# Kernel optimization log

Measured on AMD Instinct MI355X. Metric: run time of the kernel, lower is better.

Reference implementation:

```python
import jax, jax.numpy as jnp
import numpy as np

C_QKV = 1024
C_HIDDEN = 64
NUM_HEADS = 16
INF = 1e9


def setup_inputs() -> dict:
    key = jax.random.key(0)
    ks = jax.random.split(key, 10)
    B, S = 2, 2048
    d = C_QKV
    hd = C_HIDDEN * NUM_HEADS
    sc = 0.02
    return {
        "input_qkv": jax.random.normal(ks[0], (B, S, d), jnp.float32),
        "mask": jnp.ones((B, 1, 1, S), jnp.float32),
        "bias": jax.random.normal(ks[1], (1, NUM_HEADS, S, S), jnp.float32) * sc,
        "wq": jax.random.normal(ks[2], (d, hd), jnp.float32) * sc,
        "wk": jax.random.normal(ks[3], (d, hd), jnp.float32) * sc,
        "wv": jax.random.normal(ks[4], (d, hd), jnp.float32) * sc,
        "wg": jax.random.normal(ks[5], (d, hd), jnp.float32) * sc,
        "bg": jnp.zeros((hd,), jnp.float32),
        "wo": jax.random.normal(ks[6], (hd, d), jnp.float32) * sc,
        "bo": jnp.zeros((d,), jnp.float32),
    }


def reference(input_qkv, mask, bias, wq, wk, wv, wg, bg, wo, bo):
    B, S, _ = input_qkv.shape
    H, C = NUM_HEADS, C_HIDDEN
    # projections -> [B, H, S, C]
    q = (input_qkv @ wq).reshape(B, S, H, C).transpose(0, 2, 1, 3)
    k = (input_qkv @ wk).reshape(B, S, H, C).transpose(0, 2, 1, 3)
    v = (input_qkv @ wv).reshape(B, S, H, C).transpose(0, 2, 1, 3)
    q = q / jnp.asarray(C, q.dtype) ** 0.5
    # scores [B, H, S, S] with additive mask and pair bias
    a = jnp.einsum("bhqc,bhkc->bhqk", q, k)
    a = a + (mask - 1.0) * INF + bias
    a = jax.nn.softmax(a, axis=-1)
    o = jnp.einsum("bhqk,bhkc->bhqc", a, v).transpose(0, 2, 1, 3)  # [B,S,H,C]
    gate = jax.nn.sigmoid(input_qkv @ wg + bg).reshape(B, S, H, C)
    o = (o * gate).reshape(B, S, H * C)
    return o @ wo + bo
```

## Files before the change

### kernel.cpp

```cpp
#include <hip/hip_runtime.h>
#include <hip/hip_bf16.h>
#include <stdint.h>

typedef unsigned short u16;
typedef __attribute__((ext_vector_type(8))) short short8;
typedef __attribute__((ext_vector_type(4))) short short4v;
typedef __attribute__((ext_vector_type(4))) float f32x4;

#define MFMA16 __builtin_amdgcn_mfma_f32_16x16x32_bf16

#define GLOAD_LDS16(gsrc, ldst) \
  __builtin_amdgcn_global_load_lds((const __attribute__((address_space(1))) void*)(gsrc), \
                                   (__attribute__((address_space(3))) void*)(ldst), 16, 0, 0)

__device__ __forceinline__ u16 f2bf(float x) {
  union { float f; uint32_t u; } v; v.f = x;
  uint32_t r = v.u + 0x7FFFu + ((v.u >> 16) & 1u);
  return (u16)(r >> 16);
}
__device__ __forceinline__ u16 f2bf_rn(float x) {
  __hip_bfloat16 h = __float2bfloat16(x);
  return *reinterpret_cast<u16*>(&h);
}
__device__ __forceinline__ float bf2f(u16 b) {
  union { uint32_t u; float f; } v; v.u = ((uint32_t)b) << 16;
  return v.f;
}

__global__ __launch_bounds__(256) void convert_bf16_kernel(
    const float* __restrict__ in, u16* __restrict__ out, int n) {
  int i = (blockIdx.x * 256 + threadIdx.x) * 8;
  if (i >= n) return;
  float4 a = *(const float4*)(in + i);
  float4 b = *(const float4*)(in + i + 4);
  short8 t;
  t[0] = (short)f2bf(a.x); t[1] = (short)f2bf(a.y);
  t[2] = (short)f2bf(a.z); t[3] = (short)f2bf(a.w);
  t[4] = (short)f2bf(b.x); t[5] = (short)f2bf(b.y);
  t[6] = (short)f2bf(b.z); t[7] = (short)f2bf(b.w);
  *(short8*)(out + i) = t;
}

__global__ __launch_bounds__(256) void transpose_w64(
    const float* __restrict__ W, u16* __restrict__ WT, int KK, int NN) {
  __shared__ float tile[64][68];
  const int t = threadIdx.x;
  const int k0 = blockIdx.x * 64, n0 = blockIdx.y * 64;
  {
    int r = t >> 2, c0 = (t & 3) * 16;
    const float* src = W + (size_t)(k0 + r) * NN + n0 + c0;
#pragma unroll
    for (int j = 0; j < 16; j += 4) {
      float4 v = *(const float4*)(src + j);
      tile[r][c0 + j + 0] = v.x; tile[r][c0 + j + 1] = v.y;
      tile[r][c0 + j + 2] = v.z; tile[r][c0 + j + 3] = v.w;
    }
  }
  __syncthreads();
  {
    int n = t >> 2, kq = (t & 3) * 16;
    short8 t0, t1;
#pragma unroll
    for (int j = 0; j < 8; ++j)  t0[j] = (short)f2bf(tile[kq + j][n]);
#pragma unroll
    for (int j = 0; j < 8; ++j)  t1[j] = (short)f2bf(tile[kq + 8 + j][n]);
    u16* dst = WT + (size_t)(n0 + n) * KK + k0 + kq;
    *(short8*)dst = t0;
    *(short8*)(dst + 8) = t1;
  }
}

__global__ __launch_bounds__(256) void transpose_v64(
    const u16* __restrict__ vin, u16* __restrict__ vout) {
  __shared__ u16 tile[64][80];
  const int t = threadIdx.x;
  const int s0 = blockIdx.x * 64;
  const int bh = blockIdx.y;
  const int b = bh >> 4, h = bh & 15;
  {
    int r = t >> 2, c0 = (t & 3) * 16;
    const u16* src = vin + (size_t)(b * 2048 + s0 + r) * 1024 + h * 64 + c0;
    *(short8*)&tile[r][c0] = *(const short8*)src;
    *(short8*)&tile[r][c0 + 8] = *(const short8*)(src + 8);
  }
  __syncthreads();
  {
    int c = t >> 2, s4 = (t & 3) * 16;
    short8 t0, t1;
#pragma unroll
    for (int j = 0; j < 8; ++j) t0[j] = (short)tile[s4 + j][c];
#pragma unroll
    for (int j = 0; j < 8; ++j) t1[j] = (short)tile[s4 + 8 + j][c];
    u16* dst = vout + (size_t)(bh * 64 + c) * 2048 + s0 + s4;
    *(short8*)dst = t0;
    *(short8*)(dst + 8) = t1;
  }
}

__global__ __launch_bounds__(256) void gemm_bt128(
    const u16* __restrict__ A, const u16* __restrict__ BTbase,
    void* __restrict__ dstbase, const float* __restrict__ bvec, int mode) {
  const int K = 1024;
  const int tid = threadIdx.x, lane = tid & 63, w = tid >> 6;
  const int wr = w >> 1, wc = w & 1;
  const int l15 = lane & 15, lg = lane >> 4;
  const int z = (mode < 0) ? (int)blockIdx.z : mode;
  const u16* BT = (mode < 0) ? BTbase + (size_t)z * 1024 * 1024 : BTbase;
  const int rbase = blockIdx.x * 128;
  const int nbase = blockIdx.y * 128;
  __shared__ u16 lsA[128 * 64];
  __shared__ u16 lsB[128 * 64];
  f32x4 acc[4][4] = {};
  const int col8 = (lane & 7) * 8;
  for (int kt = 0; kt < K / 64; ++kt) {
#pragma unroll
    for (int i = 0; i < 4; ++i) {
      int row = w * 32 + i * 8 + (lane >> 3);
      const u16* sa = A + (size_t)(rbase + row) * K + kt * 64 + col8;
      GLOAD_LDS16(sa, lsA + (w * 32 + i * 8) * 64 + lane * 8);
      const u16* sb = BT + (size_t)(nbase + row) * K + kt * 64 + col8;
      GLOAD_LDS16(sb, lsB + (w * 32 + i * 8) * 64 + lane * 8);
    }
    __syncthreads();
#pragma unroll
    for (int kk = 0; kk < 2; ++kk) {
      short8 af[4], bfr[4];
#pragma unroll
      for (int m = 0; m < 4; ++m)
        af[m] = *(const short8*)&lsA[(wr * 64 + m * 16 + l15) * 64 + kk * 32 + lg * 8];
#pragma unroll
      for (int n = 0; n < 4; ++n)
        bfr[n] = *(const short8*)&lsB[(wc * 64 + n * 16 + l15) * 64 + kk * 32 + lg * 8];
#pragma unroll
      for (int m = 0; m < 4; ++m)
#pragma unroll
        for (int n = 0; n < 4; ++n)
          acc[m][n] = MFMA16(af[m], bfr[n], acc[m][n], 0, 0, 0);
    }
    __syncthreads();
  }
  const int r0 = rbase + wr * 64;
  const int c0 = nbase + wc * 64;
  if (z == 4) {
    float* out = (float*)dstbase;
#pragma unroll
    for (int m = 0; m < 4; ++m)
#pragma unroll
      for (int n = 0; n < 4; ++n)
#pragma unroll
        for (int i = 0; i < 4; ++i) {
          int r = r0 + m * 16 + lg * 4 + i;
          int c = c0 + n * 16 + l15;
          out[(size_t)r * 1024 + c] = acc[m][n][i] + bvec[c];
        }
  } else {
    u16* dq = (u16*)dstbase + (size_t)z * 4096 * 1024;
#pragma unroll
    for (int m = 0; m < 4; ++m)
#pragma unroll
      for (int n = 0; n < 4; ++n)
#pragma unroll
        for (int i = 0; i < 4; ++i) {
          int r = r0 + m * 16 + lg * 4 + i;
          int c = c0 + n * 16 + l15;
          float v = acc[m][n][i];
          if (z == 0) v *= 0.125f;
          else if (z == 3) v = 1.f / (1.f + __expf(-(v + bvec[c])));
          dq[(size_t)r * 1024 + c] = f2bf(v);
        }
  }
}

__global__ __launch_bounds__(256, 3) void attn_kernel(
    const u16* __restrict__ qws, const u16* __restrict__ kws,
    const u16* __restrict__ vt, const u16* __restrict__ gws,
    const float* __restrict__ bias, const float* __restrict__ mask,
    u16* __restrict__ og) {
  const int tid = threadIdx.x;
  const int lane = tid & 63;
  const int w = tid >> 6;
  const int l15 = lane & 15, lg = lane >> 4;
  const int bx = blockIdx.x;
  const int qt = (bx & 7) | ((bx >> 4) << 3);
  const int b = (bx >> 3) & 1;
  const int h = blockIdx.y;

  __shared__ __align__(16) u16 ring[3][4096];
  __shared__ __align__(16) u16 lsP[4][1280];
  __shared__ __align__(16) u16 lsM[2048];

  const float* bias_base = bias + ((size_t)h * 2048 + qt * 128) * 2048;
  const u16* vt_base = vt + (size_t)((b * 16 + h) * 64) * 2048;
  const u16* k_base = kws + (size_t)(b * 2048) * 1024 + h * 64;

  {
    float4 m0 = *(const float4*)(mask + b * 2048 + tid * 8);
    float4 m1 = *(const float4*)(mask + b * 2048 + tid * 8 + 4);
    short8 mm;
    mm[0] = (short)f2bf((m0.x - 1.f) * 1e9f); mm[1] = (short)f2bf((m0.y - 1.f) * 1e9f);
    mm[2] = (short)f2bf((m0.z - 1.f) * 1e9f); mm[3] = (short)f2bf((m0.w - 1.f) * 1e9f);
    mm[4] = (short)f2bf((m1.x - 1.f) * 1e9f); mm[5] = (short)f2bf((m1.y - 1.f) * 1e9f);
    mm[6] = (short)f2bf((m1.z - 1.f) * 1e9f); mm[7] = (short)f2bf((m1.w - 1.f) * 1e9f);
    *(short8*)&lsM[tid * 8] = mm;
  }

  const size_t qrow0 = (size_t)(b * 2048 + qt * 128 + w * 32 + l15) * 1024 + h * 64;
  const size_t qrow1 = qrow0 + 16 * 1024;
  short8 qf00 = *(const short8*)(qws + qrow0 + lg * 8);
  short8 qf01 = *(const short8*)(qws + qrow0 + 32 + lg * 8);
  short8 qf10 = *(const short8*)(qws + qrow1 + lg * 8);
  short8 qf11 = *(const short8*)(qws + qrow1 + 32 + lg * 8);
  asm volatile("" :: "v"(qf00), "v"(qf01), "v"(qf10), "v"(qf11));
  asm volatile("s_waitcnt vmcnt(0)" ::: "memory");

  f32x4 O[2][4] = {};
  float lacc0 = 0.f, lacc1 = 0.f;
  f32x4 bA0, bA1, bA2, bA3, bB0, bB1, bB2, bB3;

#define STAGE_KV(SLOT, KW) {                                                        \
    int r_ = tid >> 3, cg_ = tid & 7;                                               \
    GLOAD_LDS16(k_base + (size_t)((KW) * 32 + r_) * 1024 + ((cg_ ^ (r_ & 7)) * 8),  \
                &ring[SLOT][tid * 8]);                                              \
    int c_ = tid >> 2, kg_ = tid & 3;                                               \
    int sw_ = (c_ & 3) ^ ((c_ >> 2) & 3);                                           \
    GLOAD_LDS16(vt_base + (size_t)c_ * 2048 + (KW) * 32 + ((kg_ ^ sw_) * 8),        \
                &ring[SLOT][2048 + tid * 8]); }

#define BIAS_ISSUE(R0, R1, R2, R3, KW) {                                            \
    const float* bp_ = bias_base + (size_t)(w * 32 + l15) * 2048 + (KW) * 32 + lg * 4; \
    asm volatile("global_load_dwordx4 %0, %1, off" : "=v"(R0) : "v"(bp_));          \
    asm volatile("global_load_dwordx4 %0, %1, off" : "=v"(R1) : "v"(bp_ + 16));     \
    asm volatile("global_load_dwordx4 %0, %1, off" : "=v"(R2) : "v"(bp_ + 16 * 2048)); \
    asm volatile("global_load_dwordx4 %0, %1, off" : "=v"(R3) : "v"(bp_ + 16 * 2048 + 16)); \
  }

#define COMPUTE(SLOT, KB, BR00, BR01, BR10, BR11) {                                 \
    const u16* Kc_ = &ring[SLOT][0];                                                \
    const u16* Vc_ = &ring[SLOT][2048];                                             \
    const int sw_ = l15 & 7;                                                        \
    short8 kf0a = *(const short8*)&Kc_[(l15) * 64 + ((lg ^ sw_) * 8)];              \
    short8 kf0b = *(const short8*)&Kc_[(l15) * 64 + (((4 + lg) ^ sw_) * 8)];        \
    short8 kf1a = *(const short8*)&Kc_[(16 + l15) * 64 + ((lg ^ sw_) * 8)];         \
    short8 kf1b = *(const short8*)&Kc_[(16 + l15) * 64 + (((4 + lg) ^ sw_) * 8)];   \
    short4v mk0 = *(const short4v*)&lsM[(KB) * 32 + lg * 4];                        \
    short4v mk1 = *(const short4v*)&lsM[(KB) * 32 + 16 + lg * 4];                   \
    f32x4 ci00, ci01, ci10, ci11;                                                   \
    _Pragma("unroll") for (int i = 0; i < 4; ++i) {                                 \
      float m0_ = bf2f((u16)mk0[i]), m1_ = bf2f((u16)mk1[i]);                       \
      ci00[i] = BR00[i] + m0_; ci01[i] = BR01[i] + m1_;                             \
      ci10[i] = BR10[i] + m0_; ci11[i] = BR11[i] + m1_;                             \
    }                                                                               \
    f32x4 s00 = MFMA16(kf0a, qf00, ci00, 0, 0, 0);                                 \
    s00 = MFMA16(kf0b, qf01, s00, 0, 0, 0);                                         \
    f32x4 s01 = MFMA16(kf1a, qf00, ci01, 0, 0, 0);                                 \
    s01 = MFMA16(kf1b, qf01, s01, 0, 0, 0);                                         \
    f32x4 s10 = MFMA16(kf0a, qf10, ci10, 0, 0, 0);                                 \
    s10 = MFMA16(kf0b, qf11, s10, 0, 0, 0);                                         \
    f32x4 s11 = MFMA16(kf1a, qf10, ci11, 0, 0, 0);                                 \
    s11 = MFMA16(kf1b, qf11, s11, 0, 0, 0);                                         \
    short4v p00, p01, p10, p11;                                                     \
    _Pragma("unroll") for (int i = 0; i < 4; ++i) {                                 \
      float e00 = __expf(s00[i]); lacc0 += e00; p00[i] = (short)f2bf_rn(e00);       \
      float e01 = __expf(s01[i]); lacc0 += e01; p01[i] = (short)f2bf_rn(e01);       \
      float e10 = __expf(s10[i]); lacc1 += e10; p10[i] = (short)f2bf_rn(e10);       \
      float e11 = __expf(s11[i]); lacc1 += e11; p11[i] = (short)f2bf_rn(e11);       \
    }                                                                               \
    *(short4v*)&lsP[w][(l15) * 40 + lg * 4] = p00;                                  \
    *(short4v*)&lsP[w][(l15) * 40 + 16 + lg * 4] = p01;                             \
    *(short4v*)&lsP[w][(16 + l15) * 40 + lg * 4] = p10;                             \
    *(short4v*)&lsP[w][(16 + l15) * 40 + 16 + lg * 4] = p11;                        \
    short8 pf0 = *(const short8*)&lsP[w][(l15) * 40 + lg * 8];                      \
    short8 pf1 = *(const short8*)&lsP[w][(16 + l15) * 40 + lg * 8];                 \
    _Pragma("unroll") for (int cf = 0; cf < 4; ++cf) {                              \
      int c_ = cf * 16 + l15;                                                       \
      short8 vf_ = *(const short8*)&Vc_[c_ * 32 +                                   \
                                        ((lg ^ ((c_ & 3) ^ ((c_ >> 2) & 3))) * 8)]; \
      O[0][cf] = MFMA16(vf_, pf0, O[0][cf], 0, 0, 0);                               \
      O[1][cf] = MFMA16(vf_, pf1, O[1][cf], 0, 0, 0);                               \
    } }

#define BODY(KB, X0, X1, X2, X3, Y0, Y1, Y2, Y3) {                                  \
    if ((KB) + 2 < 64) STAGE_KV(((KB) + 2) % 3, (KB) + 2);                          \
    COMPUTE((KB) % 3, KB, X0, X1, X2, X3);                                          \
    if ((KB) + 2 < 64) {                                                            \
      BIAS_ISSUE(X0, X1, X2, X3, (KB) + 2);                                         \
      asm volatile("s_waitcnt vmcnt(6)" ::: "memory");                              \
    } else {                                                                        \
      asm volatile("s_waitcnt vmcnt(0)" ::: "memory");                              \
    }                                                                               \
    asm volatile("s_waitcnt lgkmcnt(0)" ::: "memory");                              \
    __builtin_amdgcn_sched_barrier(0);                                              \
    __builtin_amdgcn_s_barrier(); }

  STAGE_KV(0, 0);
  BIAS_ISSUE(bA0, bA1, bA2, bA3, 0);
  STAGE_KV(1, 1);
  BIAS_ISSUE(bB0, bB1, bB2, bB3, 1);
  asm volatile("s_waitcnt vmcnt(6)" ::: "memory");
  asm volatile("s_waitcnt lgkmcnt(0)" ::: "memory");
  __builtin_amdgcn_sched_barrier(0);
  __builtin_amdgcn_s_barrier();

  for (int kb2 = 0; kb2 < 64; kb2 += 2) {
    BODY(kb2,     bA0, bA1, bA2, bA3, bB0, bB1, bB2, bB3);
    BODY(kb2 + 1, bB0, bB1, bB2, bB3, bA0, bA1, bA2, bA3);
  }

  lacc0 += __shfl_xor(lacc0, 16); lacc0 += __shfl_xor(lacc0, 32);
  lacc1 += __shfl_xor(lacc1, 16); lacc1 += __shfl_xor(lacc1, 32);
  {
    float inv0 = 1.f / lacc0, inv1 = 1.f / lacc1;
#pragma unroll
    for (int cf = 0; cf < 4; ++cf) {
      short4v ga = *(const short4v*)(gws + qrow0 + cf * 16 + lg * 4);
      short4v gb = *(const short4v*)(gws + qrow1 + cf * 16 + lg * 4);
      short4v oa, ob;
#pragma unroll
      for (int i = 0; i < 4; ++i) {
        oa[i] = (short)f2bf_rn(O[0][cf][i] * inv0 * bf2f((u16)ga[i]));
        ob[i] = (short)f2bf_rn(O[1][cf][i] * inv1 * bf2f((u16)gb[i]));
      }
      *(short4v*)(og + qrow0 + cf * 16 + lg * 4) = oa;
      *(short4v*)(og + qrow1 + cf * 16 + lg * 4) = ob;
    }
  }
#undef STAGE_KV
#undef BIAS_ISSUE
#undef COMPUTE
#undef BODY
}

extern "C" void kernel_launch(void* const* d_in, const int* in_sizes, int n_in,
                              void* d_out, int out_size, void* d_ws, size_t ws_size,
                              hipStream_t stream) {
  const float* x    = (const float*)d_in[0];
  const float* mask = (const float*)d_in[1];
  const float* bias = (const float*)d_in[2];
  const float* wq   = (const float*)d_in[3];
  const float* wk   = (const float*)d_in[4];
  const float* wv   = (const float*)d_in[5];
  const float* wg   = (const float*)d_in[6];
  const float* bg   = (const float*)d_in[7];
  const float* wo   = (const float*)d_in[8];
  const float* bo   = (const float*)d_in[9];
  float* out = (float*)d_out;

  char* ws = (char*)d_ws;
  const size_t MB = 1ull << 20;
  u16* xb   = (u16*)(ws + 0);
  u16* wt   = (u16*)(ws + 8 * MB);
  u16* wot  = (u16*)(ws + 16 * MB);
  u16* proj = (u16*)(ws + 18 * MB);
  u16* vtp  = (u16*)(ws + 50 * MB);
  u16* og   = (u16*)(ws + 58 * MB);
  const size_t PSZ = (size_t)4096 * 1024;

  convert_bf16_kernel<<<2048, 256, 0, stream>>>(x, xb, 4096 * 1024);

  dim3 tg(16, 16);
  transpose_w64<<<tg, 256, 0, stream>>>(wq, wt + 0 * 1048576, 1024, 1024);
  transpose_w64<<<tg, 256, 0, stream>>>(wk, wt + 1 * 1048576, 1024, 1024);
  transpose_w64<<<tg, 256, 0, stream>>>(wv, wt + 2 * 1048576, 1024, 1024);
  transpose_w64<<<tg, 256, 0, stream>>>(wg, wt + 3 * 1048576, 1024, 1024);
  transpose_w64<<<tg, 256, 0, stream>>>(wo, wot, 1024, 1024);

  gemm_bt128<<<dim3(32, 8, 4), 256, 0, stream>>>(xb, wt, (void*)proj, bg, -1);

  transpose_v64<<<dim3(32, 32), 256, 0, stream>>>(proj + 2 * PSZ, vtp);

  attn_kernel<<<dim3(32, 16), 256, 0, stream>>>(proj, proj + PSZ, vtp, proj + 3 * PSZ,
                                                bias, mask, og);

  gemm_bt128<<<dim3(32, 8, 1), 256, 0, stream>>>(og, wot, (void*)out, bo, 4);
}
```

Baseline: 229.1 us.

## Deepen attention K/V and bias prefetch to three stages, batch weight transposes

The attention kernel's LDS ring grows from 3 to 4 slots and a third bias register set is added, so K/V tiles and bias are prefetched three blocks ahead instead of two. The vmcnt waits are retuned for the deeper pipeline, and the loop is unrolled by three with an explicit tail. Separately, the four projection-weight transposes become one launch with a z-dimension, cutting launch overhead. The extra LDS and 16 more VGPRs of bias may lower occupancy under launch_bounds(256,3).

```diff
diff --git a/kernel.cpp b/kernel.cpp
--- a/kernel.cpp
+++ b/kernel.cpp
@@ -39,6 +39,40 @@
   t[4] = (short)f2bf(b.x); t[5] = (short)f2bf(b.y);
   t[6] = (short)f2bf(b.z); t[7] = (short)f2bf(b.w);
   *(short8*)(out + i) = t;
+}
+
+__global__ __launch_bounds__(256) void transpose_w64_4(
+    const float* __restrict__ w0, const float* __restrict__ w1,
+    const float* __restrict__ w2, const float* __restrict__ w3,
+    u16* __restrict__ WT) {
+  __shared__ float tile[64][68];
+  const int t = threadIdx.x;
+  const int z = blockIdx.z;
+  const float* W = (z == 0) ? w0 : (z == 1) ? w1 : (z == 2) ? w2 : w3;
+  u16* dst_base = WT + (size_t)z * 1024 * 1024;
+  const int k0 = blockIdx.x * 64, n0 = blockIdx.y * 64;
+  {
+    int r = t >> 2, c0 = (t & 3) * 16;
+    const float* src = W + (size_t)(k0 + r) * 1024 + n0 + c0;
+#pragma unroll
+    for (int j = 0; j < 16; j += 4) {
+      float4 v = *(const float4*)(src + j);
+      tile[r][c0 + j + 0] = v.x; tile[r][c0 + j + 1] = v.y;
+      tile[r][c0 + j + 2] = v.z; tile[r][c0 + j + 3] = v.w;
+    }
+  }
+  __syncthreads();
+  {
+    int n = t >> 2, kq = (t & 3) * 16;
+    short8 t0, t1;
+#pragma unroll
+    for (int j = 0; j < 8; ++j)  t0[j] = (short)f2bf(tile[kq + j][n]);
+#pragma unroll
+    for (int j = 0; j < 8; ++j)  t1[j] = (short)f2bf(tile[kq + 8 + j][n]);
+    u16* dst = dst_base + (size_t)(n0 + n) * 1024 + k0 + kq;
+    *(short8*)dst = t0;
+    *(short8*)(dst + 8) = t1;
+  }
 }
 
 __global__ __launch_bounds__(256) void transpose_w64(
@@ -185,7 +219,7 @@
   const int b = (bx >> 3) & 1;
   const int h = blockIdx.y;
 
-  __shared__ __align__(16) u16 ring[3][4096];
+  __shared__ __align__(16) u16 ring[4][4096];
   __shared__ __align__(16) u16 lsP[4][1280];
   __shared__ __align__(16) u16 lsM[2048];
 
@@ -215,7 +249,7 @@
 
   f32x4 O[2][4] = {};
   float lacc0 = 0.f, lacc1 = 0.f;
-  f32x4 bA0, bA1, bA2, bA3, bB0, bB1, bB2, bB3;
+  f32x4 bA0, bA1, bA2, bA3, bB0, bB1, bB2, bB3, bC0, bC1, bC2, bC3;
 
 #define STAGE_KV(SLOT, KW) {                                                        \
     int r_ = tid >> 3, cg_ = tid & 7;                                               \
@@ -279,15 +313,11 @@
       O[1][cf] = MFMA16(vf_, pf1, O[1][cf], 0, 0, 0);                               \
     } }
 
-#define BODY(KB, X0, X1, X2, X3, Y0, Y1, Y2, Y3) {                                  \
-    if ((KB) + 2 < 64) STAGE_KV(((KB) + 2) % 3, (KB) + 2);                          \
-    COMPUTE((KB) % 3, KB, X0, X1, X2, X3);                                          \
-    if ((KB) + 2 < 64) {                                                            \
-      BIAS_ISSUE(X0, X1, X2, X3, (KB) + 2);                                         \
-      asm volatile("s_waitcnt vmcnt(6)" ::: "memory");                              \
-    } else {                                                                        \
-      asm volatile("s_waitcnt vmcnt(0)" ::: "memory");                              \
-    }                                                                               \
+#define BODY(KB, N, X0, X1, X2, X3) {                                               \
+    if ((KB) + 3 < 64) STAGE_KV(((KB) + 3) & 3, (KB) + 3);                          \
+    COMPUTE((KB) & 3, KB, X0, X1, X2, X3);                                          \
+    if ((KB) + 3 < 64) BIAS_ISSUE(X0, X1, X2, X3, (KB) + 3);                        \
+    asm volatile("s_waitcnt vmcnt(" #N ")" ::: "memory");                           \
     asm volatile("s_waitcnt lgkmcnt(0)" ::: "memory");                              \
     __builtin_amdgcn_sched_barrier(0);                                              \
     __builtin_amdgcn_s_barrier(); }
@@ -296,15 +326,22 @@
   BIAS_ISSUE(bA0, bA1, bA2, bA3, 0);
   STAGE_KV(1, 1);
   BIAS_ISSUE(bB0, bB1, bB2, bB3, 1);
-  asm volatile("s_waitcnt vmcnt(6)" ::: "memory");
+  STAGE_KV(2, 2);
+  BIAS_ISSUE(bC0, bC1, bC2, bC3, 2);
+  asm volatile("s_waitcnt vmcnt(12)" ::: "memory");
   asm volatile("s_waitcnt lgkmcnt(0)" ::: "memory");
   __builtin_amdgcn_sched_barrier(0);
   __builtin_amdgcn_s_barrier();
 
-  for (int kb2 = 0; kb2 < 64; kb2 += 2) {
-    BODY(kb2,     bA0, bA1, bA2, bA3, bB0, bB1, bB2, bB3);
-    BODY(kb2 + 1, bB0, bB1, bB2, bB3, bA0, bA1, bA2, bA3);
-  }
+  for (int kb3 = 0; kb3 < 60; kb3 += 3) {
+    BODY(kb3,     12, bA0, bA1, bA2, bA3);
+    BODY(kb3 + 1, 12, bB0, bB1, bB2, bB3);
+    BODY(kb3 + 2, 12, bC0, bC1, bC2, bC3);
+  }
+  BODY(60, 12, bA0, bA1, bA2, bA3);
+  BODY(61,  6, bB0, bB1, bB2, bB3);
+  BODY(62,  0, bC0, bC1, bC2, bC3);
+  BODY(63,  0, bA0, bA1, bA2, bA3);
 
   lacc0 += __shfl_xor(lacc0, 16); lacc0 += __shfl_xor(lacc0, 32);
   lacc1 += __shfl_xor(lacc1, 16); lacc1 += __shfl_xor(lacc1, 32);
@@ -357,12 +394,8 @@
 
   convert_bf16_kernel<<<2048, 256, 0, stream>>>(x, xb, 4096 * 1024);
 
-  dim3 tg(16, 16);
-  transpose_w64<<<tg, 256, 0, stream>>>(wq, wt + 0 * 1048576, 1024, 1024);
-  transpose_w64<<<tg, 256, 0, stream>>>(wk, wt + 1 * 1048576, 1024, 1024);
-  transpose_w64<<<tg, 256, 0, stream>>>(wv, wt + 2 * 1048576, 1024, 1024);
-  transpose_w64<<<tg, 256, 0, stream>>>(wg, wt + 3 * 1048576, 1024, 1024);
-  transpose_w64<<<tg, 256, 0, stream>>>(wo, wot, 1024, 1024);
+  transpose_w64_4<<<dim3(16, 16, 4), 256, 0, stream>>>(wq, wk, wv, wg, wt);
+  transpose_w64<<<dim3(16, 16), 256, 0, stream>>>(wo, wot, 1024, 1024);
 
   gemm_bt128<<<dim3(32, 8, 4), 256, 0, stream>>>(xb, wt, (void*)proj, bg, -1);
 
```

Result: faster. 224.5 us (-2.0%).
